# Kernel tuning notes

Hardware: AMD Instinct MI355X
Metric: run time of the kernel (lower is better)

Reference implementation:

```python
import jax, jax.numpy as jnp
import numpy as np

DIM = 2048
N_HEADS = 16
HEAD_DIM = DIM // N_HEADS
HIDDEN = 8192
BSZ = 2
SEQ = 2048
EPS = 1e-6


def setup_inputs() -> dict:
    key = jax.random.key(0)
    ks = jax.random.split(key, 8)
    x = jax.random.normal(ks[0], (BSZ, SEQ, DIM), dtype=jnp.float32)
    # causal additive mask, broadcastable to [B, H, S, S]
    mask = jnp.where(jnp.tril(jnp.ones((SEQ, SEQ), dtype=bool)), 0.0, -1e9)
    mask = mask[None, None, :, :].astype(jnp.float32)
    s = 0.02
    # torch.nn.Linear weights have shape [out_features, in_features]
    wq = jax.random.normal(ks[1], (DIM, DIM), dtype=jnp.float32) * s
    wk = jax.random.normal(ks[2], (DIM, DIM), dtype=jnp.float32) * s
    wv = jax.random.normal(ks[3], (DIM, DIM), dtype=jnp.float32) * s
    wo = jax.random.normal(ks[4], (DIM, DIM), dtype=jnp.float32) * s
    w1 = jax.random.normal(ks[5], (HIDDEN, DIM), dtype=jnp.float32) * s
    w2 = jax.random.normal(ks[6], (DIM, HIDDEN), dtype=jnp.float32) * s
    attn_norm_w = jnp.ones((DIM,), dtype=jnp.float32)
    ffn_norm_w = jnp.ones((DIM,), dtype=jnp.float32)
    return {"x": x, "mask": mask, "wq": wq, "wk": wk, "wv": wv, "wo": wo,
            "w1": w1, "w2": w2, "attn_norm_w": attn_norm_w, "ffn_norm_w": ffn_norm_w}


def rmsnorm(x, w):
    return x * jax.lax.rsqrt(jnp.mean(x * x, axis=-1, keepdims=True) + EPS) * w


def attention(x, mask, wq, wk, wv, wo):
    b, s, _ = x.shape
    q = (x @ wq.T).reshape(b, s, N_HEADS, HEAD_DIM)
    k = (x @ wk.T).reshape(b, s, N_HEADS, HEAD_DIM)
    v = (x @ wv.T).reshape(b, s, N_HEADS, HEAD_DIM)
    scores = jnp.einsum('bqhd,bkhd->bhqk', q, k) / jnp.sqrt(jnp.float32(HEAD_DIM))
    scores = scores + mask
    probs = jax.nn.softmax(scores, axis=-1)
    out = jnp.einsum('bhqk,bkhd->bqhd', probs, v).reshape(b, s, DIM)
    return out @ wo.T


def reference(x, mask, wq, wk, wv, wo, w1, w2, attn_norm_w, ffn_norm_w):
    h = x + attention(rmsnorm(x, attn_norm_w), mask, wq, wk, wv, wo)
    ffn_in = rmsnorm(h, ffn_norm_w)
    ffn = jax.nn.relu(ffn_in @ w1.T) @ w2.T
    return h + ffn
```

## Files before the change

### kernel.cpp

```cpp
#include <hip/hip_runtime.h>
#include <cstdint>
#include <cstddef>

#define DIM 2048
#define NHEADS 16
#define HD 128
#define HIDDEN 8192
#define BSZ 2
#define SEQ 2048
#define MTOT (BSZ*SEQ)

typedef __bf16 bf16_t;
typedef __bf16 bf16x8 __attribute__((ext_vector_type(8)));
typedef __bf16 bf16x4 __attribute__((ext_vector_type(4)));
typedef float  f32x4  __attribute__((ext_vector_type(4)));

__device__ __forceinline__ void gload16(const void* g, void* lds) {
  __builtin_amdgcn_global_load_lds(
      (const __attribute__((address_space(1))) uint32_t*)g,
      (__attribute__((address_space(3))) uint32_t*)lds, 16, 0, 0);
}

#define BAR() do { __builtin_amdgcn_sched_barrier(0); \
  asm volatile("s_barrier" ::: "memory"); \
  __builtin_amdgcn_sched_barrier(0); } while (0)
#define VMW(N) asm volatile("s_waitcnt vmcnt(" #N ")" ::: "memory")

__global__ void cvt_k(const float* __restrict__ src, bf16_t* __restrict__ dst, int n4) {
  int i = blockIdx.x * blockDim.x + threadIdx.x;
  int stride = gridDim.x * blockDim.x;
  for (; i < n4; i += stride) {
    float4 v = ((const float4*)src)[i];
    bf16x4 o = {(__bf16)v.x, (__bf16)v.y, (__bf16)v.z, (__bf16)v.w};
    ((bf16x4*)dst)[i] = o;
  }
}

__global__ __launch_bounds__(256)
void rmsnorm_k(const float* __restrict__ x, const float* __restrict__ wt,
               bf16_t* __restrict__ out) {
  const int row = blockIdx.x;
  const float* xr = x + (size_t)row * DIM;
  const int tid = threadIdx.x;
  float4 a = ((const float4*)xr)[tid];
  float4 b = ((const float4*)xr)[tid + 256];
  float ss = a.x*a.x + a.y*a.y + a.z*a.z + a.w*a.w
           + b.x*b.x + b.y*b.y + b.z*b.z + b.w*b.w;
  #pragma unroll
  for (int d = 32; d >= 1; d >>= 1) ss += __shfl_xor(ss, d, 64);
  __shared__ float red[4];
  if ((tid & 63) == 0) red[tid >> 6] = ss;
  __syncthreads();
  float tot = red[0] + red[1] + red[2] + red[3];
  float rs = rsqrtf(tot * (1.0f / DIM) + 1e-6f);
  float4 wa = ((const float4*)wt)[tid];
  float4 wb = ((const float4*)wt)[tid + 256];
  bf16x4 oa = {(__bf16)(a.x*rs*wa.x), (__bf16)(a.y*rs*wa.y),
               (__bf16)(a.z*rs*wa.z), (__bf16)(a.w*rs*wa.w)};
  bf16x4 ob = {(__bf16)(b.x*rs*wb.x), (__bf16)(b.y*rs*wb.y),
               (__bf16)(b.z*rs*wb.z), (__bf16)(b.w*rs*wb.w)};
  *(bf16x4*)(out + (size_t)row*DIM + tid*4)        = oa;
  *(bf16x4*)(out + (size_t)row*DIM + 1024 + tid*4) = ob;
}

template<int MH, int NH>
__device__ __forceinline__ void mm16(f32x4 (&acc)[8][4],
                                     const bf16x8 (&aF)[4][2],
                                     const bf16x8 (&bF)[2][2]) {
  __builtin_amdgcn_s_setprio(1);
  #pragma unroll
  for (int mt = 0; mt < 4; ++mt)
    #pragma unroll
    for (int nt = 0; nt < 2; ++nt)
      #pragma unroll
      for (int kk = 0; kk < 2; ++kk)
        acc[MH*4+mt][NH*2+nt] = __builtin_amdgcn_mfma_f32_16x16x32_bf16(
            aF[mt][kk], bF[nt][kk], acc[MH*4+mt][NH*2+nt], 0, 0, 0);
  __builtin_amdgcn_s_setprio(0);
}

__device__ __forceinline__ void rdA4(bf16x8 (&aF)[4][2], const bf16_t* rbase,
                                     int wr, int l16, int g) {
  #pragma unroll
  for (int mt = 0; mt < 4; ++mt)
    #pragma unroll
    for (int kk = 0; kk < 2; ++kk)
      aF[mt][kk] = *(const bf16x8*)((const char*)rbase +
          (wr*64 + mt*16 + l16)*128 + ((((kk<<2) ^ g) ^ (l16 & 7)) << 4));
}
__device__ __forceinline__ void rdB2(bf16x8 (&bF)[2][2], const bf16_t* rbase,
                                     int wc, int l16, int g) {
  #pragma unroll
  for (int nt = 0; nt < 2; ++nt)
    #pragma unroll
    for (int kk = 0; kk < 2; ++kk)
      bF[nt][kk] = *(const bf16x8*)((const char*)rbase +
          (wc*32 + nt*16 + l16)*128 + ((((kk<<2) ^ g) ^ (l16 & 7)) << 4));
}

template<typename OUT_T, bool RELU, bool HAS_RES, bool VT_OUT>
__global__ __launch_bounds__(512, 2)
void gemm8p(const bf16_t* __restrict__ A, const bf16_t* __restrict__ B,
            OUT_T* __restrict__ C, const float* __restrict__ res,
            int M, int N, int K) {
  __shared__ bf16_t sA[2][2][128*64];
  __shared__ bf16_t sB[2][2][128*64];
  const int tid  = threadIdx.x;
  const int lane = tid & 63;
  const int wid  = tid >> 6;
  const int l16  = lane & 15;
  const int g    = lane >> 4;
  const int wr   = wid >> 2;
  const int wc   = wid & 3;

  const int nwg = gridDim.x, bid = blockIdx.x;
  const int qq = nwg >> 3, rr = nwg & 7;
  const int xcd = bid & 7, loc = bid >> 3;
  const int wg = (xcd < rr ? xcd*(qq+1) : rr*(qq+1) + (xcd-rr)*qq) + loc;
  const int nbn = N >> 8;
  const int bm = (wg / nbn) << 8;
  const int bn = (wg % nbn) << 8;

  const int lr  = tid >> 3;
  const int cq8 = (((tid & 7) ^ (lr & 7)) << 3);

  const size_t aR = (size_t)(bm + lr) * K + cq8;
  const size_t bR = (size_t)(bn + ((lr >> 5) << 6) + (lr & 31)) * K + cq8;
  const size_t rowK128 = (size_t)128 * K, rowK64 = (size_t)64 * K, rowK32 = (size_t)32 * K;

  auto stA = [&](int buf, int mh, int kt) {
    const size_t ko = aR + (size_t)kt * 64 + (size_t)mh * rowK64;
    gload16(A + ko,            &sA[buf][mh][wid*512]);
    gload16(A + ko + rowK128,  &sA[buf][mh][4096 + wid*512]);
  };
  auto stB = [&](int buf, int nh, int kt) {
    const size_t ko = bR + (size_t)kt * 64 + (size_t)nh * rowK32;
    gload16(B + ko,              &sB[buf][nh][wid*512]);
    gload16(B + ko + 2*rowK64,   &sB[buf][nh][4096 + wid*512]);
  };

  f32x4 acc[8][4] = {};
  bf16x8 aF[4][2], bLo[2][2], bHi[2][2];

  stA(0, 0, 0); stB(0, 0, 0); stB(0, 1, 0); stA(0, 1, 0);
  stA(1, 0, 1); stB(1, 0, 1); stB(1, 1, 1);
  VMW(6);
  BAR();

  const int ni = K >> 7;
  for (int j = 0; j < ni; ++j) {
    const int t1 = 2*j + 1, t2 = 2*j + 2, t3 = 2*j + 3;
    const bool more = (j + 1 < ni);
    rdA4(aF, &sA[0][0][0], wr, l16, g);
    rdB2(bLo, &sB[0][0][0], wc, l16, g);
    stA(1, 1, t1);
    BAR();
    mm16<0,0>(acc, aF, bLo);
    BAR();
    rdB2(bHi, &sB[0][1][0], wc, l16, g);
    if (more) stA(0, 0, t2);
    BAR();
    mm16<0,1>(acc, aF, bHi);
    BAR();
    rdA4(aF, &sA[0][1][0], wr, l16, g);
    if (more) stB(0, 0, t2);
    BAR();
    mm16<1,1>(acc, aF, bHi);
    BAR();
    if (more) { stB(0, 1, t2); VMW(6); } else { VMW(0); }
    BAR();
    mm16<1,0>(acc, aF, bLo);
    BAR();
    rdA4(aF, &sA[1][0][0], wr, l16, g);
    rdB2(bLo, &sB[1][0][0], wc, l16, g);
    if (more) stA(0, 1, t2);
    BAR();
    mm16<0,0>(acc, aF, bLo);
    BAR();
    rdB2(bHi, &sB[1][1][0], wc, l16, g);
    if (more) stA(1, 0, t3);
    BAR();
    mm16<0,1>(acc, aF, bHi);
    BAR();
    rdA4(aF, &sA[1][1][0], wr, l16, g);
    if (more) stB(1, 0, t3);
    BAR();
    mm16<1,1>(acc, aF, bHi);
    BAR();
    if (more) { stB(1, 1, t3); VMW(6); }
    BAR();
    mm16<1,0>(acc, aF, bLo);
    BAR();
  }

  if (VT_OUT) {
    #pragma unroll
    for (int am = 0; am < 8; ++am) {
      const int row = bm + wr*128 + am*16 + g*4;
      #pragma unroll
      for (int an = 0; an < 4; ++an) {
        const int col = bn + wc*64 + an*16 + l16;
        f32x4 a4 = acc[am][an];
        bf16x4 v4 = {(__bf16)a4[0], (__bf16)a4[1], (__bf16)a4[2], (__bf16)a4[3]};
        *(bf16x4*)((bf16_t*)C +
            (((size_t)(row >> 11) * NHEADS + (col >> 7)) * HD + (col & 127)) * SEQ
            + (row & 2047)) = v4;
      }
    }
  } else {
    #pragma unroll
    for (int am = 0; am < 8; ++am) {
      #pragma unroll
      for (int r = 0; r < 4; ++r) {
        const int row = bm + wr*128 + am*16 + g*4 + r;
        #pragma unroll
        for (int an = 0; an < 4; ++an) {
          const int col = bn + wc*64 + an*16 + l16;
          float v = acc[am][an][r];
          if (HAS_RES) v += res[(size_t)row * N + col];
          if (RELU)    v = fmaxf(v, 0.0f);
          C[(size_t)row * N + col] = (OUT_T)v;
        }
      }
    }
  }
}

template<int MH, int NH>
__device__ __forceinline__ void mm8(f32x4 (&acc)[4][4],
                                    const bf16x8 (&aF)[2][2],
                                    const bf16x8 (&bF)[2][2]) {
  __builtin_amdgcn_s_setprio(1);
  #pragma unroll
  for (int mt = 0; mt < 2; ++mt)
    #pragma unroll
    for (int nt = 0; nt < 2; ++nt)
      #pragma unroll
      for (int kk = 0; kk < 2; ++kk)
        acc[MH*2+mt][NH*2+nt] = __builtin_amdgcn_mfma_f32_16x16x32_bf16(
            aF[mt][kk], bF[nt][kk], acc[MH*2+mt][NH*2+nt], 0, 0, 0);
  __builtin_amdgcn_s_setprio(0);
}

__device__ __forceinline__ void rd2(bf16x8 (&f)[2][2], const bf16_t* rbase,
                                    int wrow, int l16, int g) {
  #pragma unroll
  for (int t = 0; t < 2; ++t)
    #pragma unroll
    for (int kk = 0; kk < 2; ++kk)
      f[t][kk] = *(const bf16x8*)((const char*)rbase +
          (wrow + t*16 + l16)*128 + ((((kk<<2) ^ g) ^ (l16 & 7)) << 4));
}

template<typename OUT_T, bool RELU, bool HAS_RES, bool VT_OUT>
__global__ __launch_bounds__(512, 2)
void gemm8p_n128(const bf16_t* __restrict__ A, const bf16_t* __restrict__ B,
                 OUT_T* __restrict__ C, const float* __restrict__ res,
                 int M, int N, int K) {
  __shared__ bf16_t sA[2][2][128*64];
  __shared__ bf16_t sB[2][2][64*64];
  const int tid  = threadIdx.x;
  const int lane = tid & 63;
  const int wid  = tid >> 6;
  const int l16  = lane & 15;
  const int g    = lane >> 4;
  const int wr   = wid >> 1;
  const int wc   = wid & 1;

  const int nwg = gridDim.x, bid = blockIdx.x;
  const int qq = nwg >> 3, rr = nwg & 7;
  const int xcd = bid & 7, loc = bid >> 3;
  const int wg = (xcd < rr ? xcd*(qq+1) : rr*(qq+1) + (xcd-rr)*qq) + loc;
  const int nbn = N >> 7;
  const int bm = (wg / nbn) << 8;
  const int bn = (wg % nbn) << 7;

  const int lr  = tid >> 3;
  const int cq8 = (((tid & 7) ^ (lr & 7)) << 3);
  const size_t aR = (size_t)(bm + ((lr >> 5) << 6) + (lr & 31)) * K + cq8;
  const size_t bR = (size_t)(bn + ((lr >> 5) << 6) + (lr & 31)) * K + cq8;
  const size_t rowK128 = (size_t)128 * K, rowK32 = (size_t)32 * K;

  auto stA = [&](int buf, int mh, int kt) {
    const size_t ko = aR + (size_t)kt * 64 + (size_t)mh * rowK32;
    gload16(A + ko,            &sA[buf][mh][wid*512]);
    gload16(A + ko + rowK128,  &sA[buf][mh][4096 + wid*512]);
  };
  auto stB = [&](int buf, int nh, int kt) {
    gload16(B + bR + (size_t)kt * 64 + (size_t)nh * rowK32, &sB[buf][nh][wid*512]);
  };

  f32x4 acc[4][4] = {};
  bf16x8 aF[2][2], bLo[2][2], bHi[2][2];

  stA(0, 0, 0); stB(0, 0, 0); stB(0, 1, 0); stA(0, 1, 0);
  stA(1, 0, 1); stB(1, 0, 1); stB(1, 1, 1);
  VMW(4);
  BAR();

  const int ar = wr*32;
  const int br = wc*32;
  const int ni = K >> 7;
  for (int j = 0; j < ni; ++j) {
    const int t1 = 2*j + 1, t2 = 2*j + 2, t3 = 2*j + 3;
    const bool more = (j + 1 < ni);
    rd2(aF,  &sA[0][0][0], ar, l16, g);
    rd2(bLo, &sB[0][0][0], br, l16, g);
    stA(1, 1, t1);
    BAR();
    mm8<0,0>(acc, aF, bLo);
    BAR();
    rd2(bHi, &sB[0][1][0], br, l16, g);
    if (more) stA(0, 0, t2);
    BAR();
    mm8<0,1>(acc, aF, bHi);
    BAR();
    rd2(aF, &sA[0][1][0], ar, l16, g);
    if (more) stB(0, 0, t2);
    BAR();
    mm8<1,1>(acc, aF, bHi);
    BAR();
    if (more) { stB(0, 1, t2); VMW(4); } else { VMW(0); }
    BAR();
    mm8<1,0>(acc, aF, bLo);
    BAR();
    rd2(aF,  &sA[1][0][0], ar, l16, g);
    rd2(bLo, &sB[1][0][0], br, l16, g);
    if (more) stA(0, 1, t2);
    BAR();
    mm8<0,0>(acc, aF, bLo);
    BAR();
    rd2(bHi, &sB[1][1][0], br, l16, g);
    if (more) stA(1, 0, t3);
    BAR();
    mm8<0,1>(acc, aF, bHi);
    BAR();
    rd2(aF, &sA[1][1][0], ar, l16, g);
    if (more) stB(1, 0, t3);
    BAR();
    mm8<1,1>(acc, aF, bHi);
    BAR();
    if (more) { stB(1, 1, t3); VMW(4); }
    BAR();
    mm8<1,0>(acc, aF, bLo);
    BAR();
  }

  if (VT_OUT) {
    #pragma unroll
    for (int am = 0; am < 4; ++am) {
      const int row = bm + wr*64 + am*16 + g*4;
      #pragma unroll
      for (int an = 0; an < 4; ++an) {
        const int col = bn + wc*64 + an*16 + l16;
        f32x4 a4 = acc[am][an];
        bf16x4 v4 = {(__bf16)a4[0], (__bf16)a4[1], (__bf16)a4[2], (__bf16)a4[3]};
        *(bf16x4*)((bf16_t*)C +
            (((size_t)(row >> 11) * NHEADS + (col >> 7)) * HD + (col & 127)) * SEQ
            + (row & 2047)) = v4;
      }
    }
  } else {
    #pragma unroll
    for (int am = 0; am < 4; ++am) {
      #pragma unroll
      for (int r = 0; r < 4; ++r) {
        const int row = bm + wr*64 + am*16 + g*4 + r;
        #pragma unroll
        for (int an = 0; an < 4; ++an) {
          const int col = bn + wc*64 + an*16 + l16;
          float v = acc[am][an][r];
          if (HAS_RES) v += res[(size_t)row * N + col];
          if (RELU)    v = fmaxf(v, 0.0f);
          C[(size_t)row * N + col] = (OUT_T)v;
        }
      }
    }
  }
}

__global__ __launch_bounds__(256, 2)
void attn_k(const bf16_t* __restrict__ Q, const bf16_t* __restrict__ Kk,
            const bf16_t* __restrict__ VT, bf16_t* __restrict__ O) {
  __shared__ bf16_t sK[2][64 * 128];
  __shared__ bf16_t sVT[2][128 * 64];
  __shared__ bf16_t sP[4][32 * 64];
  const int tid = threadIdx.x, lane = tid & 63, w = tid >> 6;
  const int l16 = lane & 15, g = lane >> 4;
  const int b = blockIdx.z, h = blockIdx.y;
  const int qt = b ? (SEQ/128 - 1 - blockIdx.x) : blockIdx.x;
  const int ch = h * HD;
  const size_t gb = (size_t)b * SEQ * DIM;
  const int qbase = qt*128 + w*32;
  const bf16_t* VTh = VT + ((size_t)b * NHEADS + h) * ((size_t)HD * SEQ);

  bf16x8 qf[2][4];
  #pragma unroll
  for (int mt = 0; mt < 2; ++mt)
    #pragma unroll
    for (int kb = 0; kb < 4; ++kb)
      qf[mt][kb] = *(const bf16x8*)(Q + gb + (size_t)(qbase + mt*16 + l16)*DIM + ch + kb*32 + g*8);

  f32x4 o[2][8] = {};
  float m_r[2][4], l_r[2][4];
  #pragma unroll
  for (int mt = 0; mt < 2; ++mt)
    #pragma unroll
    for (int r = 0; r < 4; ++r) { m_r[mt][r] = -1e9f; l_r[mt][r] = 0.0f; }

  const float rs = 0.08838834764831845f;
  const int nsteps = (qt*128 + 128) >> 6;

  auto stageK = [&](int buf, int kv0) {
    #pragma unroll
    for (int i = 0; i < 4; ++i) {
      const int c = i*256 + tid;
      const int kv = c >> 4, pos = c & 15;
      const int qsrc = pos ^ (kv & 7);
      gload16(Kk + gb + (size_t)(kv0 + kv)*DIM + ch + (qsrc << 3),
              (char*)sK[buf] + (size_t)(i*256 + w*64)*16);
    }
  };
  auto stageVT = [&](int buf, int kv0) {
    #pragma unroll
    for (int i = 0; i < 4; ++i) {
      const int c = i*256 + tid;
      const int d = c >> 3, p = c & 7;
      const int q = p ^ (d & 7);
      gload16(VTh + (size_t)d * SEQ + kv0 + (q << 3),
              (char*)sVT[buf] + (size_t)(i*256 + w*64)*16);
    }
  };

  stageK(0, 0);  stageVT(0, 0);
  if (nsteps > 1) { stageK(1, 64); stageVT(1, 64); }
  __syncthreads();

  int cur = 0;
  for (int t = 0; t < nsteps; ++t) {
    const int kv0 = t << 6;
    const bool active = (kv0 < qbase + 32);
    if (active) {
      f32x4 s[2][4] = {};
      const char* kb_ = (const char*)sK[cur];
      #pragma unroll
      for (int nt = 0; nt < 4; ++nt) {
        const int row = nt*16 + l16;
        #pragma unroll
        for (int kbi = 0; kbi < 4; ++kbi) {
          const int pos = (kbi*4 + g) ^ (l16 & 7);
          bf16x8 kf = *(const bf16x8*)(kb_ + row*256 + (pos << 4));
          #pragma unroll
          for (int mt = 0; mt < 2; ++mt)
            s[mt][nt] = __builtin_amdgcn_mfma_f32_16x16x32_bf16(qf[mt][kbi], kf, s[mt][nt], 0, 0, 0);
        }
      }

      const bool needmask = (kv0 + 63 > qbase);
      char* pb = (char*)sP[w];
      #pragma unroll
      for (int mt = 0; mt < 2; ++mt) {
        #pragma unroll
        for (int r = 0; r < 4; ++r) {
          const int qpos = qbase + mt*16 + g*4 + r;
          float sv[4];
          #pragma unroll
          for (int nt = 0; nt < 4; ++nt) {
            sv[nt] = s[mt][nt][r] * rs;
            if (needmask && (kv0 + nt*16 + l16 > qpos)) sv[nt] = -1e9f;
          }
          float mx = fmaxf(fmaxf(sv[0], sv[1]), fmaxf(sv[2], sv[3]));
          #pragma unroll
          for (int d = 8; d >= 1; d >>= 1) mx = fmaxf(mx, __shfl_xor(mx, d, 16));
          const float mo = m_r[mt][r];
          if (mx > mo) {
            const float sc = __expf(mo - mx);
            l_r[mt][r] *= sc;
            #pragma unroll
            for (int dt = 0; dt < 8; ++dt) o[mt][dt][r] *= sc;
            m_r[mt][r] = mx;
          }
          const float mn = m_r[mt][r];
          float p[4], rsum = 0.0f;
          #pragma unroll
          for (int nt = 0; nt < 4; ++nt) { p[nt] = __expf(sv[nt] - mn); rsum += p[nt]; }
          #pragma unroll
          for (int d = 8; d >= 1; d >>= 1) rsum += __shfl_xor(rsum, d, 16);
          l_r[mt][r] += rsum;
          const int prow = mt*16 + g*4 + r;
          #pragma unroll
          for (int nt = 0; nt < 4; ++nt)
            *(bf16_t*)(pb + ((prow*128 + nt*32 + l16*2) ^ (g << 5))) = (bf16_t)p[nt];
        }
      }

      bf16x8 pa[2][2];
      #pragma unroll
      for (int mt = 0; mt < 2; ++mt) {
        const int row2 = mt*16 + l16;
        #pragma unroll
        for (int ks = 0; ks < 2; ++ks)
          pa[mt][ks] = *(const bf16x8*)((const char*)sP[w] +
                    ((row2*128 + ks*64 + g*16) ^ (((l16 >> 2) & 3) << 5)));
      }

      const char* vb_ = (const char*)sVT[cur];
      #pragma unroll
      for (int dt = 0; dt < 8; ++dt) {
        const int d = dt*16 + l16;
        #pragma unroll
        for (int ks = 0; ks < 2; ++ks) {
          const int pos = (ks*4 + g) ^ (d & 7);
          bf16x8 vf = *(const bf16x8*)(vb_ + d*128 + (pos << 4));
          #pragma unroll
          for (int mt = 0; mt < 2; ++mt)
            o[mt][dt] = __builtin_amdgcn_mfma_f32_16x16x32_bf16(pa[mt][ks], vf, o[mt][dt], 0, 0, 0);
        }
      }
    }
    __syncthreads();
    if (t + 2 < nsteps) {
      stageK(cur, (t + 2) << 6);
      stageVT(cur, (t + 2) << 6);
    }
    cur ^= 1;
  }

  #pragma unroll
  for (int mt = 0; mt < 2; ++mt) {
    #pragma unroll
    for (int r = 0; r < 4; ++r) {
      const float inv = 1.0f / l_r[mt][r];
      const int row = qbase + mt*16 + g*4 + r;
      #pragma unroll
      for (int dt = 0; dt < 8; ++dt)
        O[gb + (size_t)row*DIM + ch + dt*16 + l16] = (bf16_t)(o[mt][dt][r] * inv);
    }
  }
}

extern "C" void kernel_launch(void* const* d_in, const int* in_sizes, int n_in,
                              void* d_out, int out_size, void* d_ws, size_t ws_size,
                              hipStream_t stream) {
  const float* x   = (const float*)d_in[0];
  const float* wq  = (const float*)d_in[2];
  const float* wk  = (const float*)d_in[3];
  const float* wv  = (const float*)d_in[4];
  const float* wo  = (const float*)d_in[5];
  const float* w1  = (const float*)d_in[6];
  const float* w2  = (const float*)d_in[7];
  const float* anw = (const float*)d_in[8];
  const float* fnw = (const float*)d_in[9];
  float* out = (float*)d_out;

  char* p = (char*)d_ws;
  bf16_t* wqb = (bf16_t*)p; p += (size_t)DIM*DIM*2;
  bf16_t* wkb = (bf16_t*)p; p += (size_t)DIM*DIM*2;
  bf16_t* wvb = (bf16_t*)p; p += (size_t)DIM*DIM*2;
  bf16_t* wob = (bf16_t*)p; p += (size_t)DIM*DIM*2;
  bf16_t* w1b = (bf16_t*)p; p += (size_t)DIM*HIDDEN*2;
  bf16_t* w2b = (bf16_t*)p; p += (size_t)DIM*HIDDEN*2;
  bf16_t* xn  = (bf16_t*)p; p += (size_t)MTOT*DIM*2;
  float*  hb  = (float*)p;  p += (size_t)MTOT*DIM*4;
  bf16_t* big = (bf16_t*)p; p += (size_t)MTOT*HIDDEN*2;
  bf16_t* qb = big;
  bf16_t* kb = big + (size_t)MTOT*DIM;
  bf16_t* vT = big + 2*(size_t)MTOT*DIM;
  bf16_t* ab = big + 3*(size_t)MTOT*DIM;
  bf16_t* f1 = big;

  auto cvt = [&](const float* s, bf16_t* d, size_t n) {
    int n4 = (int)(n / 4);
    int blocks = (n4 + 255) / 256; if (blocks > 4096) blocks = 4096;
    cvt_k<<<blocks, 256, 0, stream>>>(s, d, n4);
  };
  cvt(wq, wqb, (size_t)DIM*DIM);
  cvt(wk, wkb, (size_t)DIM*DIM);
  cvt(wv, wvb, (size_t)DIM*DIM);
  cvt(wo, wob, (size_t)DIM*DIM);
  cvt(w1, w1b, (size_t)DIM*HIDDEN);
  cvt(w2, w2b, (size_t)DIM*HIDDEN);

  rmsnorm_k<<<MTOT, 256, 0, stream>>>(x, anw, xn);

  gemm8p_n128<bf16_t, false, false, false><<<256, 512, 0, stream>>>(xn, wqb, qb, nullptr, MTOT, DIM, DIM);
  gemm8p_n128<bf16_t, false, false, false><<<256, 512, 0, stream>>>(xn, wkb, kb, nullptr, MTOT, DIM, DIM);
  gemm8p_n128<bf16_t, false, false, true ><<<256, 512, 0, stream>>>(xn, wvb, vT, nullptr, MTOT, DIM, DIM);

  attn_k<<<dim3(SEQ/128, NHEADS, BSZ), 256, 0, stream>>>(qb, kb, vT, ab);

  gemm8p_n128<float, false, true, false><<<256, 512, 0, stream>>>(ab, wob, hb, x, MTOT, DIM, DIM);

  rmsnorm_k<<<MTOT, 256, 0, stream>>>(hb, fnw, xn);

  gemm8p<bf16_t, true, false, false><<<512, 512, 0, stream>>>(xn, w1b, f1, nullptr, MTOT, HIDDEN, DIM);

  gemm8p_n128<float, false, true, false><<<256, 512, 0, stream>>>(f1, w2b, out, hb, MTOT, DIM, HIDDEN);
}
```

Before: 657.1 us.

## Replace ping-pong GEMM with triple-buffered 64-wide K pipeline

Replaces the N=128 GEMM's two-buffer, quarter-tile schedule with a three-stage LDS ring of full 256x64 A and 128x64 B tiles, prefetching two K-steps ahead. Each wave reads four A and four B fragments per half K-step and issues a 4x4 MFMA block, with fewer barriers per K-step. This aims to hide global load latency and cut synchronisation overhead, at the cost of more LDS (144KB) that limits occupancy to one block per CU.

Result: slower. 680.6 us (+3.6%).

```diff
diff --git a/kernel.cpp b/kernel.cpp
--- a/kernel.cpp
+++ b/kernel.cpp
@@ -226,39 +226,25 @@
   }
 }
 
-template<int MH, int NH>
-__device__ __forceinline__ void mm8(f32x4 (&acc)[4][4],
-                                    const bf16x8 (&aF)[2][2],
-                                    const bf16x8 (&bF)[2][2]) {
+__device__ __forceinline__ void mmN(f32x4 (&acc)[4][4],
+                                    const bf16x8 (&aF)[4], const bf16x8 (&bF)[4]) {
   __builtin_amdgcn_s_setprio(1);
   #pragma unroll
-  for (int mt = 0; mt < 2; ++mt)
-    #pragma unroll
-    for (int nt = 0; nt < 2; ++nt)
-      #pragma unroll
-      for (int kk = 0; kk < 2; ++kk)
-        acc[MH*2+mt][NH*2+nt] = __builtin_amdgcn_mfma_f32_16x16x32_bf16(
-            aF[mt][kk], bF[nt][kk], acc[MH*2+mt][NH*2+nt], 0, 0, 0);
+  for (int mt = 0; mt < 4; ++mt)
+    #pragma unroll
+    for (int nt = 0; nt < 4; ++nt)
+      acc[mt][nt] = __builtin_amdgcn_mfma_f32_16x16x32_bf16(
+          aF[mt], bF[nt], acc[mt][nt], 0, 0, 0);
   __builtin_amdgcn_s_setprio(0);
-}
-
-__device__ __forceinline__ void rd2(bf16x8 (&f)[2][2], const bf16_t* rbase,
-                                    int wrow, int l16, int g) {
-  #pragma unroll
-  for (int t = 0; t < 2; ++t)
-    #pragma unroll
-    for (int kk = 0; kk < 2; ++kk)
-      f[t][kk] = *(const bf16x8*)((const char*)rbase +
-          (wrow + t*16 + l16)*128 + ((((kk<<2) ^ g) ^ (l16 & 7)) << 4));
 }
 
 template<typename OUT_T, bool RELU, bool HAS_RES, bool VT_OUT>
 __global__ __launch_bounds__(512, 2)
-void gemm8p_n128(const bf16_t* __restrict__ A, const bf16_t* __restrict__ B,
-                 OUT_T* __restrict__ C, const float* __restrict__ res,
-                 int M, int N, int K) {
-  __shared__ bf16_t sA[2][2][128*64];
-  __shared__ bf16_t sB[2][2][64*64];
+void gemm3b(const bf16_t* __restrict__ A, const bf16_t* __restrict__ B,
+            OUT_T* __restrict__ C, const float* __restrict__ res,
+            int M, int N, int K) {
+  __shared__ bf16_t sA[3][256*64];
+  __shared__ bf16_t sB[3][128*64];
   const int tid  = threadIdx.x;
   const int lane = tid & 63;
   const int wid  = tid >> 6;
@@ -275,75 +261,67 @@
   const int bm = (wg / nbn) << 8;
   const int bn = (wg % nbn) << 7;
 
-  const int lr  = tid >> 3;
-  const int cq8 = (((tid & 7) ^ (lr & 7)) << 3);
-  const size_t aR = (size_t)(bm + ((lr >> 5) << 6) + (lr & 31)) * K + cq8;
-  const size_t bR = (size_t)(bn + ((lr >> 5) << 6) + (lr & 31)) * K + cq8;
-  const size_t rowK128 = (size_t)128 * K, rowK32 = (size_t)32 * K;
-
-  auto stA = [&](int buf, int mh, int kt) {
-    const size_t ko = aR + (size_t)kt * 64 + (size_t)mh * rowK32;
-    gload16(A + ko,            &sA[buf][mh][wid*512]);
-    gload16(A + ko + rowK128,  &sA[buf][mh][4096 + wid*512]);
-  };
-  auto stB = [&](int buf, int nh, int kt) {
-    gload16(B + bR + (size_t)kt * 64 + (size_t)nh * rowK32, &sB[buf][nh][wid*512]);
+  auto stA2 = [&](int buf, int kt, int half) {
+    #pragma unroll
+    for (int i = half*2; i < half*2 + 2; ++i) {
+      const int c = i*512 + tid;
+      const int row = c >> 3;
+      const int q = (c & 7) ^ (row & 7);
+      gload16(A + (size_t)(bm + row) * K + kt*64 + q*8,
+              (char*)sA[buf] + (size_t)(i*512 + wid*64) * 16);
+    }
+  };
+  auto stB1 = [&](int buf, int kt, int half) {
+    const int c = half*512 + tid;
+    const int row = c >> 3;
+    const int q = (c & 7) ^ (row & 7);
+    gload16(B + (size_t)(bn + row) * K + kt*64 + q*8,
+            (char*)sB[buf] + (size_t)(half*512 + wid*64) * 16);
+  };
+  auto rdA = [&](bf16x8 (&aF)[4], const bf16_t* base, int kh) {
+    #pragma unroll
+    for (int mt = 0; mt < 4; ++mt) {
+      const int row = wr*64 + mt*16 + l16;
+      aF[mt] = *(const bf16x8*)((const char*)base +
+               row*128 + ((((kh<<2) + g) ^ (l16 & 7)) << 4));
+    }
+  };
+  auto rdB = [&](bf16x8 (&bF)[4], const bf16_t* base, int kh) {
+    #pragma unroll
+    for (int nt = 0; nt < 4; ++nt) {
+      const int row = wc*64 + nt*16 + l16;
+      bF[nt] = *(const bf16x8*)((const char*)base +
+               row*128 + ((((kh<<2) + g) ^ (l16 & 7)) << 4));
+    }
   };
 
   f32x4 acc[4][4] = {};
-  bf16x8 aF[2][2], bLo[2][2], bHi[2][2];
-
-  stA(0, 0, 0); stB(0, 0, 0); stB(0, 1, 0); stA(0, 1, 0);
-  stA(1, 0, 1); stB(1, 0, 1); stB(1, 1, 1);
-  VMW(4);
+
+  stA2(0, 0, 0); stA2(0, 0, 1); stB1(0, 0, 0); stB1(0, 0, 1);
+  stA2(1, 1, 0); stA2(1, 1, 1); stB1(1, 1, 0); stB1(1, 1, 1);
+  VMW(6);
   BAR();
 
-  const int ar = wr*32;
-  const int br = wc*32;
-  const int ni = K >> 7;
-  for (int j = 0; j < ni; ++j) {
-    const int t1 = 2*j + 1, t2 = 2*j + 2, t3 = 2*j + 3;
-    const bool more = (j + 1 < ni);
-    rd2(aF,  &sA[0][0][0], ar, l16, g);
-    rd2(bLo, &sB[0][0][0], br, l16, g);
-    stA(1, 1, t1);
-    BAR();
-    mm8<0,0>(acc, aF, bLo);
-    BAR();
-    rd2(bHi, &sB[0][1][0], br, l16, g);
-    if (more) stA(0, 0, t2);
-    BAR();
-    mm8<0,1>(acc, aF, bHi);
-    BAR();
-    rd2(aF, &sA[0][1][0], ar, l16, g);
-    if (more) stB(0, 0, t2);
-    BAR();
-    mm8<1,1>(acc, aF, bHi);
-    BAR();
-    if (more) { stB(0, 1, t2); VMW(4); } else { VMW(0); }
-    BAR();
-    mm8<1,0>(acc, aF, bLo);
-    BAR();
-    rd2(aF,  &sA[1][0][0], ar, l16, g);
-    rd2(bLo, &sB[1][0][0], br, l16, g);
-    if (more) stA(0, 1, t2);
-    BAR();
-    mm8<0,0>(acc, aF, bLo);
-    BAR();
-    rd2(bHi, &sB[1][1][0], br, l16, g);
-    if (more) stA(1, 0, t3);
-    BAR();
-    mm8<0,1>(acc, aF, bHi);
-    BAR();
-    rd2(aF, &sA[1][1][0], ar, l16, g);
-    if (more) stB(1, 0, t3);
-    BAR();
-    mm8<1,1>(acc, aF, bHi);
-    BAR();
-    if (more) { stB(1, 1, t3); VMW(4); }
-    BAR();
-    mm8<1,0>(acc, aF, bLo);
-    BAR();
+  const int nk = K >> 6;
+  int bcur = 0;
+  for (int t = 0; t < nk; ++t) {
+    const int bnx = (bcur >= 1) ? bcur - 1 : 2;
+    const bool pf = (t + 2 < nk);
+    bf16x8 aF[4], bF[4];
+    rdA(aF, sA[bcur], 0);
+    rdB(bF, sB[bcur], 0);
+    if (pf) { stA2(bnx, t+2, 0); stB1(bnx, t+2, 0); }
+    BAR();
+    mmN(acc, aF, bF);
+    BAR();
+    rdA(aF, sA[bcur], 1);
+    rdB(bF, sB[bcur], 1);
+    if (pf) { stA2(bnx, t+2, 1); stB1(bnx, t+2, 1); }
+    BAR();
+    mmN(acc, aF, bF);
+    if (pf) { VMW(6); } else { VMW(0); }
+    BAR();
+    bcur = (bcur == 2) ? 0 : bcur + 1;
   }
 
   if (VT_OUT) {
@@ -583,17 +561,17 @@
 
   rmsnorm_k<<<MTOT, 256, 0, stream>>>(x, anw, xn);
 
-  gemm8p_n128<bf16_t, false, false, false><<<256, 512, 0, stream>>>(xn, wqb, qb, nullptr, MTOT, DIM, DIM);
-  gemm8p_n128<bf16_t, false, false, false><<<256, 512, 0, stream>>>(xn, wkb, kb, nullptr, MTOT, DIM, DIM);
-  gemm8p_n128<bf16_t, false, false, true ><<<256, 512, 0, stream>>>(xn, wvb, vT, nullptr, MTOT, DIM, DIM);
+  gemm3b<bf16_t, false, false, false><<<256, 512, 0, stream>>>(xn, wqb, qb, nullptr, MTOT, DIM, DIM);
+  gemm3b<bf16_t, false, false, false><<<256, 512, 0, stream>>>(xn, wkb, kb, nullptr, MTOT, DIM, DIM);
+  gemm3b<bf16_t, false, false, true ><<<256, 512, 0, stream>>>(xn, wvb, vT, nullptr, MTOT, DIM, DIM);
 
   attn_k<<<dim3(SEQ/128, NHEADS, BSZ), 256, 0, stream>>>(qb, kb, vT, ab);
 
-  gemm8p_n128<float, false, true, false><<<256, 512, 0, stream>>>(ab, wob, hb, x, MTOT, DIM, DIM);
+  gemm3b<float, false, true, false><<<256, 512, 0, stream>>>(ab, wob, hb, x, MTOT, DIM, DIM);
 
   rmsnorm_k<<<MTOT, 256, 0, stream>>>(hb, fnw, xn);
 
   gemm8p<bf16_t, true, false, false><<<512, 512, 0, stream>>>(xn, w1b, f1, nullptr, MTOT, HIDDEN, DIM);
 
-  gemm8p_n128<float, false, true, false><<<256, 512, 0, stream>>>(f1, w2b, out, hb, MTOT, DIM, HIDDEN);
-}
+  gemm3b<float, false, true, false><<<256, 512, 0, stream>>>(f1, w2b, out, hb, MTOT, DIM, HIDDEN);
+}
```
